# Performance work log

Measured on AMD Instinct MI355X. Metric: run time of the kernel, lower is better.

## Reference

```python
import jax, jax.numpy as jnp
import numpy as np

N = 50000
E = 600000
IN, HID, OUT = 128, 128, 64
EPS = 1e-5

def setup_inputs() -> dict:
    key = jax.random.key(0)
    ks = jax.random.split(key, 16)
    def lin(k, i, o):
        s = 1.0 / np.sqrt(i)
        return jax.random.uniform(k, (i, o), jnp.float32, -s, s)
    inp = {
        "x": jax.random.normal(ks[0], (N, IN), jnp.float32),
        "edge_index": jax.random.randint(ks[1], (2, E), 0, N, jnp.int32),
        "edge_weight": jax.random.uniform(ks[2], (E,), jnp.float32),
        # SAGEConv params: lin_l (aggregated neighbors, with bias), lin_r (root)
        "Wl0": lin(ks[3], IN, HID), "Wr0": lin(ks[4], IN, HID), "b0": jnp.zeros((HID,), jnp.float32),
        "Wl1": lin(ks[5], HID, HID), "Wr1": lin(ks[6], HID, HID), "b1": jnp.zeros((HID,), jnp.float32),
        "Wl2": lin(ks[7], HID, OUT), "Wr2": lin(ks[8], HID, OUT), "b2": jnp.zeros((OUT,), jnp.float32),
        "gamma0": jnp.ones((HID,), jnp.float32), "beta0": jnp.zeros((HID,), jnp.float32),
        "gamma1": jnp.ones((HID,), jnp.float32), "beta1": jnp.zeros((HID,), jnp.float32),
    }
    return inp

def _sage_conv(x, src, dst, w, Wl, Wr, b):
    # weighted message m_e = w_e * x[src_e], mean-aggregated at dst
    msg = x[src] * w[:, None]                                   # [E, F]
    agg = jax.ops.segment_sum(msg, dst, num_segments=N)          # [N, F]
    cnt = jax.ops.segment_sum(jnp.ones_like(w), dst, num_segments=N)
    mean = agg / jnp.maximum(cnt, 1.0)[:, None]
    return mean @ Wl + b + x @ Wr

def _bn(x, gamma, beta):
    mu = jnp.mean(x, axis=0)
    var = jnp.var(x, axis=0)
    return (x - mu) * jax.lax.rsqrt(var + EPS) * gamma + beta

def reference(x, edge_index, edge_weight,
              Wl0, Wr0, b0, Wl1, Wr1, b1, Wl2, Wr2, b2,
              gamma0, beta0, gamma1, beta1):
    src, dst = edge_index[0], edge_index[1]
    h = _sage_conv(x, src, dst, edge_weight, Wl0, Wr0, b0)
    h = jax.nn.relu(_bn(h, gamma0, beta0))  # dropout: identity in eval
    h = _sage_conv(h, src, dst, edge_weight, Wl1, Wr1, b1)
    h = jax.nn.relu(_bn(h, gamma1, beta1))
    return _sage_conv(h, src, dst, edge_weight, Wl2, Wr2, b2)
```

## Files before the change

kernel.cpp:

```cpp
#include <hip/hip_runtime.h>
#include <hip/hip_bf16.h>

#define NN 50000
#define EE 600000
#define SREP 64
#define SCB 49

typedef short bf16x8 __attribute__((ext_vector_type(8)));
typedef float f32x4 __attribute__((ext_vector_type(4)));

__device__ inline ushort f2bf(float x) {
  unsigned u = __float_as_uint(x);
  u = (u + 0x7fffu + ((u >> 16) & 1u)) >> 16;
  return (ushort)u;
}
__device__ inline float bflo(uint t) { return __uint_as_float(t << 16); }
__device__ inline float bfhi(uint t) { return __uint_as_float(t & 0xffff0000u); }
__device__ inline uint f22bf(float a, float b) { return ((uint)f2bf(b) << 16) | (uint)f2bf(a); }

#define EB 2344

__global__ void prep0_k(const int* __restrict__ ei, int* __restrict__ cnt_d,
                        const float* __restrict__ Wl0, const float* __restrict__ Wr0,
                        const float* __restrict__ Wl1, const float* __restrict__ Wr1,
                        const float* __restrict__ Wl2, const float* __restrict__ Wr2,
                        ushort* __restrict__ wbuf) {
  const int b = blockIdx.x;
  if (b < EB) {
    int e = b * 256 + threadIdx.x;
    if (e < EE) atomicAdd(&cnt_d[ei[EE + e]], 1);
  } else {
    int idx = (b - EB) * 256 + threadIdx.x;
    const float* W; int F, r, off;
    if (idx < 16384)      { W = Wl0; F = 128; r = idx;         off = 0; }
    else if (idx < 32768) { W = Wr0; F = 128; r = idx - 16384; off = 16384; }
    else if (idx < 49152) { W = Wl1; F = 128; r = idx - 32768; off = 32768; }
    else if (idx < 65536) { W = Wr1; F = 128; r = idx - 49152; off = 49152; }
    else if (idx < 73728) { W = Wl2; F = 64;  r = idx - 65536; off = 65536; }
    else                  { W = Wr2; F = 64;  r = idx - 73728; off = 73728; }
    int k = r / F, n = r % F;
    wbuf[off + n * 128 + ((((k >> 3) + n) & 15) << 3) + (k & 7)] = f2bf(W[k * F + n]);
  }
}

__global__ __launch_bounds__(256) void scanA_k(const int* __restrict__ cnt,
                                               int* __restrict__ cur,
                                               int* __restrict__ bsum) {
  __shared__ int ls[256];
  const int t = threadIdx.x;
  const int base = blockIdx.x * 1024 + t * 4;
  int4 v = {0, 0, 0, 0};
  if (base + 3 < NN) v = *(const int4*)(cnt + base);
  else {
    if (base + 0 < NN) v.x = cnt[base + 0];
    if (base + 1 < NN) v.y = cnt[base + 1];
    if (base + 2 < NN) v.z = cnt[base + 2];
  }
  ls[t] = v.x + v.y + v.z + v.w;
  __syncthreads();
  for (int off = 1; off < 256; off <<= 1) {
    int u = (t >= off) ? ls[t - off] : 0;
    __syncthreads();
    ls[t] += u;
    __syncthreads();
  }
  int ex = (t == 0) ? 0 : ls[t - 1];
  int4 o;
  o.x = ex;
  o.y = ex + v.x;
  o.z = o.y + v.y;
  o.w = o.z + v.z;
  if (base + 3 < NN) *(int4*)(cur + base) = o;
  else {
    if (base + 0 < NN) cur[base + 0] = o.x;
    if (base + 1 < NN) cur[base + 1] = o.y;
    if (base + 2 < NN) cur[base + 2] = o.z;
  }
  if (t == 255) bsum[blockIdx.x] = ls[255];
}

__global__ __launch_bounds__(256) void scanC_k(int* __restrict__ cur,
                                               const int* __restrict__ bsum,
                                               const int* __restrict__ cnt_d,
                                               int* __restrict__ rowp,
                                               float* __restrict__ invd) {
  __shared__ int soff;
  const int t = threadIdx.x;
  if (t < 64) {
    int own = (t < SCB) ? bsum[t] : 0;
    int v = own;
#pragma unroll
    for (int o = 1; o < 64; o <<= 1) {
      int u = __shfl_up(v, o, 64);
      if (t >= o) v += u;
    }
    int incl = __shfl(v, blockIdx.x, 64);
    int ownb = __shfl(own, blockIdx.x, 64);
    if (t == 0) soff = incl - ownb;
  }
  __syncthreads();
  const int off = soff;
  const int base = blockIdx.x * 1024 + t * 4;
  if (base + 3 < NN) {
    int4 v = *(int4*)(cur + base);
    v.x += off; v.y += off; v.z += off; v.w += off;
    *(int4*)(cur + base) = v;
    *(int4*)(rowp + base) = v;
    int4 cd = *(const int4*)(cnt_d + base);
    float4 iv;
    iv.x = 1.0f / (float)max(cd.x, 1);
    iv.y = 1.0f / (float)max(cd.y, 1);
    iv.z = 1.0f / (float)max(cd.z, 1);
    iv.w = 1.0f / (float)max(cd.w, 1);
    *(float4*)(invd + base) = iv;
  } else {
    for (int i = 0; i < 4; ++i) {
      if (base + i < NN) {
        int v = cur[base + i] + off;
        cur[base + i] = v;
        rowp[base + i] = v;
        invd[base + i] = 1.0f / (float)max(cnt_d[base + i], 1);
      }
    }
  }
}

__global__ void fill_k(const int* __restrict__ ei, const float* __restrict__ ew,
                       int* __restrict__ cur_d, int2* __restrict__ eL) {
  int e = blockIdx.x * 256 + threadIdx.x;
  if (e < EE) {
    int s = ei[e], d = ei[EE + e];
    int pc = atomicAdd(&cur_d[d], 1);
    int2 v;
    v.x = s;
    v.y = __float_as_int(ew[e]);
    eL[pc] = v;
  }
}

template <int F, bool HB16>
__global__ __launch_bounds__(256) void gemm_mfma(
    const void* __restrict__ H, const ushort* __restrict__ Wpre,
    const float* __restrict__ statsb, const float* __restrict__ gamma,
    const float* __restrict__ beta, ushort* __restrict__ Tlb,
    ushort* __restrict__ Trb) {
  __shared__ __align__(16) ushort Wt[F * 128];
  __shared__ float ssl[256];
  const int tid = threadIdx.x;
  const int lane = tid & 63;
  const int w = tid >> 6;
  const int col = lane & 15;
  const int quad = lane >> 4;
  const int nb = blockIdx.x * 128;

  if (HB16) {
    float s = 0.f;
#pragma unroll 8
    for (int r = 0; r < SREP; ++r) s += statsb[r * 256 + tid];
    ssl[tid] = s;
    __syncthreads();
    if (tid < 128) {
      float mu = ssl[tid] * (1.0f / (float)NN);
      float ex2 = ssl[128 + tid] * (1.0f / (float)NN);
      float var = ex2 - mu * mu;
      float sc = gamma[tid] * rsqrtf(var + 1e-5f);
      ssl[tid] = sc;
      ssl[128 + tid] = beta[tid] - mu * sc;
    }
    __syncthreads();
  }

  bf16x8 afrag[2][4];
#pragma unroll
  for (int t2 = 0; t2 < 2; ++t2) {
    const int row = nb + w * 32 + t2 * 16 + col;
#pragma unroll
    for (int s = 0; s < 4; ++s) {
      const int c = s * 4 + quad;
      const int gk = c * 8;
      uint4 hv = {0, 0, 0, 0};
      if (HB16) {
        if (row < NN) hv = *(const uint4*)((const ushort*)H + (size_t)row * 128 + gk);
        uint* p = (uint*)&hv;
#pragma unroll
        for (int j = 0; j < 4; ++j) {
          float f0 = fmaxf(fmaf(bflo(p[j]), ssl[gk + 2 * j], ssl[128 + gk + 2 * j]), 0.f);
          float f1 = fmaxf(fmaf(bfhi(p[j]), ssl[gk + 2 * j + 1], ssl[128 + gk + 2 * j + 1]), 0.f);
          p[j] = f22bf(f0, f1);
        }
      } else {
        float4 fa = {0.f, 0.f, 0.f, 0.f}, fb = {0.f, 0.f, 0.f, 0.f};
        if (row < NN) {
          fa = *(const float4*)((const float*)H + (size_t)row * 128 + gk);
          fb = *(const float4*)((const float*)H + (size_t)row * 128 + gk + 4);
        }
        uint* p = (uint*)&hv;
        p[0] = f22bf(fa.x, fa.y);
        p[1] = f22bf(fa.z, fa.w);
        p[2] = f22bf(fb.x, fb.y);
        p[3] = f22bf(fb.z, fb.w);
      }
      afrag[t2][s] = *(const bf16x8*)&hv;
    }
  }

  for (int phase = 0; phase < 2; ++phase) {
    const uint4* src = (const uint4*)(Wpre + phase * F * 128);
    __syncthreads();
    for (int i = tid; i < F * 16; i += 256) ((uint4*)Wt)[i] = src[i];
    __syncthreads();
    ushort* Outp = phase ? Trb : Tlb;
#pragma unroll 2
    for (int ct = 0; ct < F / 16; ++ct) {
      const int n = ct * 16 + col;
      f32x4 acc0 = {0.f, 0.f, 0.f, 0.f};
      f32x4 acc1 = {0.f, 0.f, 0.f, 0.f};
#pragma unroll
      for (int s = 0; s < 4; ++s) {
        const int c = s * 4 + quad;
        bf16x8 b = *(const bf16x8*)&Wt[n * 128 + (((c + n) & 15) << 3)];
        acc0 = __builtin_amdgcn_mfma_f32_16x16x32_bf16(afrag[0][s], b, acc0, 0, 0, 0);
        acc1 = __builtin_amdgcn_mfma_f32_16x16x32_bf16(afrag[1][s], b, acc1, 0, 0, 0);
      }
      const int cc = ct * 16 + col;
      const int nodeb0 = nb + w * 32 + quad * 4;
#pragma unroll
      for (int r = 0; r < 4; ++r) {
        const int node = nodeb0 + r;
        if (node < NN) Outp[(size_t)node * F + cc] = f2bf(acc0[r]);
      }
#pragma unroll
      for (int r = 0; r < 4; ++r) {
        const int node = nodeb0 + 16 + r;
        if (node < NN) Outp[(size_t)node * F + cc] = f2bf(acc1[r]);
      }
    }
  }
}

template <int F, bool STATS, bool OUTF32>
__global__ __launch_bounds__(256, 8) void gather_combine(
    const ushort* __restrict__ Tlb, const int2* __restrict__ eL,
    const int* __restrict__ rowp, const int* __restrict__ cnt_d,
    const ushort* __restrict__ Trb, const float* __restrict__ invd,
    const float* __restrict__ bias, void* __restrict__ outp,
    float* __restrict__ statsb) {
  constexpr int L = F / 2;
  constexpr int NPI = 256 / L;
  constexpr int NPB = (L == 64) ? 20 : 16;
  const int tid = threadIdx.x;
  const int cp = tid % L;
  const int c = 2 * cp;
  const int nl = tid / L;
  const int n0 = blockIdx.x * NPB;
  const float bx = bias[c], by = bias[c + 1];
  float2 S = {0.f, 0.f}, Q = {0.f, 0.f};
#pragma unroll
  for (int it = 0; it < NPB / NPI; ++it) {
    int n = n0 + it * NPI + nl;
    if constexpr (L == 64) n = __builtin_amdgcn_readfirstlane(n);
    const int beg = rowp[n];
    const int deg = cnt_d[n];
    float a0 = 0.f, a1 = 0.f;
    for (int base = 0; base < deg; base += L) {
      const int take = deg - base;
      int2 er = {0, 0};
      if (cp < take) er = eL[beg + base + cp];
      int m = take < L ? take : L;
      if constexpr (L == 32) m = max(m, __shfl_xor(m, 32, 64));
      int j = 0;
      for (; j + 4 <= m; j += 4) {
        int s0 = __shfl(er.x, j + 0, L);
        int s1 = __shfl(er.x, j + 1, L);
        int s2 = __shfl(er.x, j + 2, L);
        int s3 = __shfl(er.x, j + 3, L);
        float w0 = __int_as_float(__shfl(er.y, j + 0, L));
        float w1 = __int_as_float(__shfl(er.y, j + 1, L));
        float w2 = __int_as_float(__shfl(er.y, j + 2, L));
        float w3 = __int_as_float(__shfl(er.y, j + 3, L));
        uint t0 = ((const uint*)Tlb)[(size_t)s0 * L + cp];
        uint t1 = ((const uint*)Tlb)[(size_t)s1 * L + cp];
        uint t2 = ((const uint*)Tlb)[(size_t)s2 * L + cp];
        uint t3 = ((const uint*)Tlb)[(size_t)s3 * L + cp];
        a0 = fmaf(w0, bflo(t0), a0); a1 = fmaf(w0, bfhi(t0), a1);
        a0 = fmaf(w1, bflo(t1), a0); a1 = fmaf(w1, bfhi(t1), a1);
        a0 = fmaf(w2, bflo(t2), a0); a1 = fmaf(w2, bfhi(t2), a1);
        a0 = fmaf(w3, bflo(t3), a0); a1 = fmaf(w3, bfhi(t3), a1);
      }
      for (; j < m; ++j) {
        int s0 = __shfl(er.x, j, L);
        float w0 = __int_as_float(__shfl(er.y, j, L));
        uint t0 = ((const uint*)Tlb)[(size_t)s0 * L + cp];
        a0 = fmaf(w0, bflo(t0), a0);
        a1 = fmaf(w0, bfhi(t0), a1);
      }
    }
    float iv = invd[n];
    uint tb = ((const uint*)Trb)[(size_t)n * L + cp];
    float2 v;
    v.x = fmaf(a0, iv, bflo(tb) + bx);
    v.y = fmaf(a1, iv, bfhi(tb) + by);
    if (OUTF32) *(float2*)((float*)outp + (size_t)n * F + c) = v;
    else ((uint*)outp)[(size_t)n * L + cp] = f22bf(v.x, v.y);
    if constexpr (STATS) {
      S.x += v.x; S.y += v.y;
      Q.x += v.x * v.x; Q.y += v.y * v.y;
    }
  }
  if constexpr (STATS) {
    __shared__ float2 sS[4][L];
    __shared__ float2 sQ[4][L];
    const int wid = tid >> 6, wl = tid & 63;
    if constexpr (L == 64) {
      sS[wid][wl] = S;
      sQ[wid][wl] = Q;
    } else {
      S.x += __shfl_xor(S.x, 32, 64); S.y += __shfl_xor(S.y, 32, 64);
      Q.x += __shfl_xor(Q.x, 32, 64); Q.y += __shfl_xor(Q.y, 32, 64);
      if (wl < 32) { sS[wid][wl] = S; sQ[wid][wl] = Q; }
    }
    __syncthreads();
    if (tid < L) {
      float2 Sa = sS[0][tid], Qa = sQ[0][tid];
#pragma unroll
      for (int w2 = 1; w2 < 4; ++w2) {
        Sa.x += sS[w2][tid].x; Sa.y += sS[w2][tid].y;
        Qa.x += sQ[w2][tid].x; Qa.y += sQ[w2][tid].y;
      }
      float* sb = statsb + (size_t)(blockIdx.x & (SREP - 1)) * 256;
      int col = 2 * tid;
      atomicAdd(&sb[col], Sa.x);
      atomicAdd(&sb[col + 1], Sa.y);
      atomicAdd(&sb[128 + col], Qa.x);
      atomicAdd(&sb[128 + col + 1], Qa.y);
    }
  }
}

extern "C" void kernel_launch(void* const* d_in, const int* in_sizes, int n_in,
                              void* d_out, int out_size, void* d_ws, size_t ws_size,
                              hipStream_t stream) {
  (void)in_sizes; (void)n_in; (void)out_size; (void)ws_size;
  const float* x   = (const float*)d_in[0];
  const int*   ei  = (const int*)d_in[1];
  const float* ew  = (const float*)d_in[2];
  const float* Wl0 = (const float*)d_in[3];
  const float* Wr0 = (const float*)d_in[4];
  const float* b0  = (const float*)d_in[5];
  const float* Wl1 = (const float*)d_in[6];
  const float* Wr1 = (const float*)d_in[7];
  const float* b1  = (const float*)d_in[8];
  const float* Wl2 = (const float*)d_in[9];
  const float* Wr2 = (const float*)d_in[10];
  const float* b2  = (const float*)d_in[11];
  const float* g0  = (const float*)d_in[12];
  const float* be0 = (const float*)d_in[13];
  const float* g1  = (const float*)d_in[14];
  const float* be1 = (const float*)d_in[15];
  float* out = (float*)d_out;

  size_t off = 0;
  auto alloc = [&](size_t b) -> void* {
    void* p = (char*)d_ws + off;
    off += (b + 255) & ~(size_t)255;
    return p;
  };
  ushort* tlb  = (ushort*)alloc((size_t)NN * 128 * 2);
  ushort* trb  = (ushort*)alloc((size_t)NN * 128 * 2);
  ushort* hpre = (ushort*)alloc((size_t)NN * 128 * 2);
  int2* eL     = (int2*)alloc((size_t)EE * 8);
  ushort* wbuf = (ushort*)alloc(81920 * 2);
  const size_t CNT_B  = ((size_t)NN * 4 + 255) & ~(size_t)255;
  const size_t STAT_B = (size_t)SREP * 256 * 4;
  char* zb = (char*)alloc(CNT_B + 2 * STAT_B);
  int*   cnt_d   = (int*)zb;
  float* statsb0 = (float*)(zb + CNT_B);
  float* statsb1 = (float*)(zb + CNT_B + STAT_B);
  int*  cur_d  = (int*)alloc((size_t)NN * 4);
  int*  rowp   = (int*)alloc((size_t)NN * 4);
  int*  bsum   = (int*)alloc(SCB * 4);
  float* invd  = (float*)alloc((size_t)NN * 4);

  const int GEMMB = (NN + 127) / 128;
  const int GB128 = NN / 20;
  const int GB64  = NN / 16;

  hipMemsetAsync(zb, 0, CNT_B + 2 * STAT_B, stream);
  prep0_k<<<EB + 320, 256, 0, stream>>>(ei, cnt_d, Wl0, Wr0, Wl1, Wr1, Wl2, Wr2, wbuf);
  scanA_k<<<SCB, 256, 0, stream>>>(cnt_d, cur_d, bsum);
  scanC_k<<<SCB, 256, 0, stream>>>(cur_d, bsum, cnt_d, rowp, invd);
  fill_k<<<EB, 256, 0, stream>>>(ei, ew, cur_d, eL);

  gemm_mfma<128, false><<<GEMMB, 256, 0, stream>>>(x, wbuf, nullptr, nullptr, nullptr, tlb, trb);
  gather_combine<128, true, false><<<GB128, 256, 0, stream>>>(tlb, eL, rowp, cnt_d, trb, invd, b0, hpre, statsb0);

  gemm_mfma<128, true><<<GEMMB, 256, 0, stream>>>(hpre, wbuf + 32768, statsb0, g0, be0, tlb, trb);
  gather_combine<128, true, false><<<GB128, 256, 0, stream>>>(tlb, eL, rowp, cnt_d, trb, invd, b1, hpre, statsb1);

  gemm_mfma<64, true><<<GEMMB, 256, 0, stream>>>(hpre, wbuf + 65536, statsb1, g1, be1, tlb, trb);
  gather_combine<64, false, true><<<GB64, 256, 0, stream>>>(tlb, eL, rowp, cnt_d, trb, invd, b2, out, nullptr);
}
```

Baseline: 303.2 us.

## Split GEMM blocks by weight phase and halve rows per block

The node-feature GEMM previously had each block compute 128 rows against both the neighbor and root weight matrices in sequence. Now each block handles 64 rows and a single weight matrix, chosen from the block index, which raises the grid from about 391 to about 1564 blocks for better CU occupancy. The weight load into shared memory now overlaps with the activation loads. In exchange, input rows and the batch-norm prologue are read and computed twice, once per phase. The stats replication factor also drops from 64 to 16, reducing the per-block stats reduction at the cost of more atomic contention when the stats are accumulated.

```diff
diff --git a/kernel.cpp b/kernel.cpp
--- a/kernel.cpp
+++ b/kernel.cpp
@@ -3,7 +3,7 @@
 
 #define NN 50000
 #define EE 600000
-#define SREP 64
+#define SREP 16
 #define SCB 49
 
 typedef short bf16x8 __attribute__((ext_vector_type(8)));
@@ -151,7 +151,8 @@
   const int w = tid >> 6;
   const int col = lane & 15;
   const int quad = lane >> 4;
-  const int nb = blockIdx.x * 128;
+  const int phase = blockIdx.x & 1;
+  const int nb = (blockIdx.x >> 1) * 64;
 
   if (HB16) {
     float s = 0.f;
@@ -170,70 +171,60 @@
     __syncthreads();
   }
 
-  bf16x8 afrag[2][4];
-#pragma unroll
-  for (int t2 = 0; t2 < 2; ++t2) {
-    const int row = nb + w * 32 + t2 * 16 + col;
+  {
+    const uint4* src = (const uint4*)(Wpre + (size_t)phase * F * 128);
+    for (int i = tid; i < F * 16; i += 256) ((uint4*)Wt)[i] = src[i];
+  }
+
+  bf16x8 afrag[4];
+  const int row = nb + w * 16 + col;
+#pragma unroll
+  for (int s = 0; s < 4; ++s) {
+    const int c = s * 4 + quad;
+    const int gk = c * 8;
+    uint4 hv = {0, 0, 0, 0};
+    if (HB16) {
+      if (row < NN) hv = *(const uint4*)((const ushort*)H + (size_t)row * 128 + gk);
+      uint* p = (uint*)&hv;
+#pragma unroll
+      for (int j = 0; j < 4; ++j) {
+        float f0 = fmaxf(fmaf(bflo(p[j]), ssl[gk + 2 * j], ssl[128 + gk + 2 * j]), 0.f);
+        float f1 = fmaxf(fmaf(bfhi(p[j]), ssl[gk + 2 * j + 1], ssl[128 + gk + 2 * j + 1]), 0.f);
+        p[j] = f22bf(f0, f1);
+      }
+    } else {
+      float4 fa = {0.f, 0.f, 0.f, 0.f}, fb = {0.f, 0.f, 0.f, 0.f};
+      if (row < NN) {
+        fa = *(const float4*)((const float*)H + (size_t)row * 128 + gk);
+        fb = *(const float4*)((const float*)H + (size_t)row * 128 + gk + 4);
+      }
+      uint* p = (uint*)&hv;
+      p[0] = f22bf(fa.x, fa.y);
+      p[1] = f22bf(fa.z, fa.w);
+      p[2] = f22bf(fb.x, fb.y);
+      p[3] = f22bf(fb.z, fb.w);
+    }
+    afrag[s] = *(const bf16x8*)&hv;
+  }
+
+  __syncthreads();
+  ushort* Outp = phase ? Trb : Tlb;
+  const int nodeb = nb + w * 16 + quad * 4;
+#pragma unroll 2
+  for (int ct = 0; ct < F / 16; ++ct) {
+    const int n = ct * 16 + col;
+    f32x4 acc = {0.f, 0.f, 0.f, 0.f};
 #pragma unroll
     for (int s = 0; s < 4; ++s) {
       const int c = s * 4 + quad;
-      const int gk = c * 8;
-      uint4 hv = {0, 0, 0, 0};
-      if (HB16) {
-        if (row < NN) hv = *(const uint4*)((const ushort*)H + (size_t)row * 128 + gk);
-        uint* p = (uint*)&hv;
-#pragma unroll
-        for (int j = 0; j < 4; ++j) {
-          float f0 = fmaxf(fmaf(bflo(p[j]), ssl[gk + 2 * j], ssl[128 + gk + 2 * j]), 0.f);
-          float f1 = fmaxf(fmaf(bfhi(p[j]), ssl[gk + 2 * j + 1], ssl[128 + gk + 2 * j + 1]), 0.f);
-          p[j] = f22bf(f0, f1);
-        }
-      } else {
-        float4 fa = {0.f, 0.f, 0.f, 0.f}, fb = {0.f, 0.f, 0.f, 0.f};
-        if (row < NN) {
-          fa = *(const float4*)((const float*)H + (size_t)row * 128 + gk);
-          fb = *(const float4*)((const float*)H + (size_t)row * 128 + gk + 4);
-        }
-        uint* p = (uint*)&hv;
-        p[0] = f22bf(fa.x, fa.y);
-        p[1] = f22bf(fa.z, fa.w);
-        p[2] = f22bf(fb.x, fb.y);
-        p[3] = f22bf(fb.z, fb.w);
-      }
-      afrag[t2][s] = *(const bf16x8*)&hv;
-    }
-  }
-
-  for (int phase = 0; phase < 2; ++phase) {
-    const uint4* src = (const uint4*)(Wpre + phase * F * 128);
-    __syncthreads();
-    for (int i = tid; i < F * 16; i += 256) ((uint4*)Wt)[i] = src[i];
-    __syncthreads();
-    ushort* Outp = phase ? Trb : Tlb;
-#pragma unroll 2
-    for (int ct = 0; ct < F / 16; ++ct) {
-      const int n = ct * 16 + col;
-      f32x4 acc0 = {0.f, 0.f, 0.f, 0.f};
-      f32x4 acc1 = {0.f, 0.f, 0.f, 0.f};
-#pragma unroll
-      for (int s = 0; s < 4; ++s) {
-        const int c = s * 4 + quad;
-        bf16x8 b = *(const bf16x8*)&Wt[n * 128 + (((c + n) & 15) << 3)];
-        acc0 = __builtin_amdgcn_mfma_f32_16x16x32_bf16(afrag[0][s], b, acc0, 0, 0, 0);
-        acc1 = __builtin_amdgcn_mfma_f32_16x16x32_bf16(afrag[1][s], b, acc1, 0, 0, 0);
-      }
-      const int cc = ct * 16 + col;
-      const int nodeb0 = nb + w * 32 + quad * 4;
-#pragma unroll
-      for (int r = 0; r < 4; ++r) {
-        const int node = nodeb0 + r;
-        if (node < NN) Outp[(size_t)node * F + cc] = f2bf(acc0[r]);
-      }
-#pragma unroll
-      for (int r = 0; r < 4; ++r) {
-        const int node = nodeb0 + 16 + r;
-        if (node < NN) Outp[(size_t)node * F + cc] = f2bf(acc1[r]);
-      }
+      bf16x8 b = *(const bf16x8*)&Wt[n * 128 + (((c + n) & 15) << 3)];
+      acc = __builtin_amdgcn_mfma_f32_16x16x32_bf16(afrag[s], b, acc, 0, 0, 0);
+    }
+    const int cc = ct * 16 + col;
+#pragma unroll
+    for (int r = 0; r < 4; ++r) {
+      const int node = nodeb + r;
+      if (node < NN) Outp[(size_t)node * F + cc] = f2bf(acc[r]);
     }
   }
 }
@@ -381,7 +372,7 @@
   int*  bsum   = (int*)alloc(SCB * 4);
   float* invd  = (float*)alloc((size_t)NN * 4);
 
-  const int GEMMB = (NN + 127) / 128;
+  const int GEMMB = 2 * ((NN + 63) / 64);
   const int GB128 = NN / 20;
   const int GB64  = NN / 16;
 
```

Measured after the change: 306.4 us. About the same (+1.1%).
